# Kernel optimization log

Measured on AMD Instinct MI355X. Metric: run time of the kernel, lower is better.

The kernel has to match this reference:

```python
import math
import jax, jax.numpy as jnp
import numpy as np

B, S, CNN_D, LLM_D, BR_D, H = 4, 1024, 512, 768, 1024, 16
PW, CW = 0.2, 0.15  # physics_weight, conservation_weight


def _ln(x, g, b, eps=1e-5):
    m = jnp.mean(x, axis=-1, keepdims=True)
    v = jnp.var(x, axis=-1, keepdims=True)
    return (x - m) * jax.lax.rsqrt(v + eps) * g + b


def _mha(x, wqkv, bqkv, wo, bo, h=H):
    # torch nn.MultiheadAttention (batch_first, self-attention, eval mode)
    Bb, Ss, E = x.shape
    d = E // h
    qkv = x @ wqkv.T + bqkv
    q, k, v = jnp.split(qkv, 3, axis=-1)
    sh = lambda t: t.reshape(Bb, Ss, h, d).transpose(0, 2, 1, 3)
    q, k, v = sh(q), sh(k), sh(v)
    a = jax.nn.softmax(jnp.einsum('bhqd,bhkd->bhqk', q, k) / math.sqrt(d), axis=-1)
    o = jnp.einsum('bhqk,bhkd->bhqd', a, v).transpose(0, 2, 1, 3).reshape(Bb, Ss, E)
    return o @ wo.T + bo


def _phys_attn(qx, kx, wq, bq, wk, bk, wv, bv, wo, bo, g, be, h=H):
    # PhysicsInformedAttention._physics_attention (requires Sq == Sk for the bias broadcast)
    Bb, Sq, E = qx.shape
    Sk = kx.shape[1]
    d = E // h
    Q = (qx @ wq.T + bq).reshape(Bb, Sq, h, d).transpose(0, 2, 1, 3)
    K = (kx @ wk.T + bk).reshape(Bb, Sk, h, d).transpose(0, 2, 1, 3)
    V = (kx @ wv.T + bv).reshape(Bb, Sk, h, d).transpose(0, 2, 1, 3)
    scores = jnp.einsum('bhqd,bhkd->bhqk', Q, K) / math.sqrt(d)
    energy_bias = jnp.sum(Q * K, axis=-1, keepdims=True) * PW   # [B,H,S,1]
    mass_bias = jnp.mean(Q + K, axis=-1, keepdims=True) * CW    # [B,H,S,1]
    a = jax.nn.softmax(scores + energy_bias + mass_bias, axis=-1)
    o = jnp.einsum('bhqk,bhkd->bhqd', a, V).transpose(0, 2, 1, 3).reshape(Bb, Sq, E)
    return _ln(qx + (o @ wo.T + bo), g, be)


def _bridge(x, w, b, g, be):
    # Linear -> GELU (exact) -> LayerNorm (Dropout is no-op in eval)
    return _ln(jax.nn.gelu(x @ w.T + b, approximate=False), g, be)


def setup_inputs() -> dict:
    key = jax.random.key(0)
    ks = iter(jax.random.split(key, 64))
    nrm = lambda *s: jax.random.normal(next(ks), s, jnp.float32)
    w = lambda *s: nrm(*s) * 0.02
    return dict(
        datacube=nrm(B, 5, 8, 16, 16),
        llm_features=nrm(B, S, LLM_D),
        enhanced_cnn_features=nrm(B, S, CNN_D),
        sa_wqkv=w(3 * CNN_D, CNN_D), sa_bqkv=jnp.zeros(3 * CNN_D),
        sa_wo=w(CNN_D, CNN_D), sa_bo=jnp.zeros(CNN_D),
        ta_wqkv=w(3 * CNN_D, CNN_D), ta_bqkv=jnp.zeros(3 * CNN_D),
        ta_wo=w(CNN_D, CNN_D), ta_bo=jnp.zeros(CNN_D),
        c2b_w=w(BR_D, CNN_D), c2b_b=jnp.zeros(BR_D), c2b_g=jnp.ones(BR_D), c2b_be=jnp.zeros(BR_D),
        l2b_w=w(BR_D, LLM_D), l2b_b=jnp.zeros(BR_D), l2b_g=jnp.ones(BR_D), l2b_be=jnp.zeros(BR_D),
        pq_w=w(BR_D, BR_D), pq_b=jnp.zeros(BR_D),
        pk_w=w(BR_D, BR_D), pk_b=jnp.zeros(BR_D),
        pv_w=w(BR_D, BR_D), pv_b=jnp.zeros(BR_D),
        po_w=w(BR_D, BR_D), po_b=jnp.zeros(BR_D),
        e_emb=nrm(1, 1, BR_D), m_emb=nrm(1, 1, BR_D), p_emb=nrm(1, 1, BR_D),
        pa_g=jnp.ones(BR_D), pa_be=jnp.zeros(BR_D),
        c2l_w=w(LLM_D, BR_D), c2l_b=jnp.zeros(LLM_D), c2l_g=jnp.ones(LLM_D), c2l_be=jnp.zeros(LLM_D),
        l2c_w=w(CNN_D, BR_D), l2c_b=jnp.zeros(CNN_D), l2c_g=jnp.ones(CNN_D), l2c_be=jnp.zeros(CNN_D),
    )


def reference(datacube, llm_features, enhanced_cnn_features,
              sa_wqkv, sa_bqkv, sa_wo, sa_bo,
              ta_wqkv, ta_bqkv, ta_wo, ta_bo,
              c2b_w, c2b_b, c2b_g, c2b_be,
              l2b_w, l2b_b, l2b_g, l2b_be,
              pq_w, pq_b, pk_w, pk_b, pv_w, pv_b, po_w, po_b,
              e_emb, m_emb, p_emb, pa_g, pa_be,
              c2l_w, c2l_b, c2l_g, c2l_be,
              l2c_w, l2c_b, l2c_g, l2c_be):
    # enhanced_cnn_features path bypasses the conv3d processor
    cnn = enhanced_cnn_features                       # [B,S,512]
    cnn = cnn + _mha(cnn, sa_wqkv, sa_bqkv, sa_wo, sa_bo)   # spatial integration
    cnn = cnn + _mha(cnn, ta_wqkv, ta_bqkv, ta_wo, ta_bo)   # temporal integration
    cnn_b = _bridge(cnn, c2b_w, c2b_b, c2b_g, c2b_be)       # [B,S,1024]
    llm_b = _bridge(llm_features, l2b_w, l2b_b, l2b_g, l2b_be)  # [B,S,1024]
    phys = jnp.broadcast_to(jnp.concatenate([e_emb, m_emb, p_emb], axis=1),
                            (cnn.shape[0], 3, BR_D))
    aug_cnn = jnp.concatenate([cnn_b, phys], axis=1)  # [B,S+3,1024]
    aug_llm = jnp.concatenate([llm_b, phys], axis=1)
    cnn_att = _phys_attn(aug_cnn, aug_llm, pq_w, pq_b, pk_w, pk_b, pv_w, pv_b,
                         po_w, po_b, pa_g, pa_be)[:, :S]
    llm_att = _phys_attn(aug_llm, aug_cnn, pq_w, pq_b, pk_w, pk_b, pv_w, pv_b,
                         po_w, po_b, pa_g, pa_be)[:, :S]
    llm_enhanced = _bridge(cnn_att, c2l_w, c2l_b, c2l_g, c2l_be)  # cnn->llm bridge [B,S,768]
    cnn_enhanced = _bridge(llm_att, l2c_w, l2c_b, l2c_g, l2c_be)  # llm->cnn bridge [B,S,512]
    return (cnn_enhanced, llm_enhanced)
```

## Files before the change

kernel.cpp:

```cpp
#include <hip/hip_runtime.h>
#include <cstdint>
#include <cstddef>

#define B_    4
#define S_    1024
#define CNN_DIM 512
#define LLM_DIM 768
#define BR_DIM  1024
#define NH    16
#define SAUG  1027

typedef __attribute__((ext_vector_type(8))) short short8;
typedef __attribute__((ext_vector_type(4))) float f32x4;
typedef __attribute__((ext_vector_type(4))) unsigned short us4;
typedef unsigned short u16;
typedef unsigned int u32;
typedef unsigned long long u64;

__device__ __forceinline__ float bf2f(u16 h) {
    union { u32 u; float f; } c; c.u = ((u32)h) << 16; return c.f;
}
__device__ __forceinline__ u16 f2bf(float f) {
    union { u32 u; float f; } c; c.f = f;
    return (u16)((c.u + 0x7FFFu + ((c.u >> 16) & 1u)) >> 16);
}
__device__ __forceinline__ short f2bfS(float f) { return (short)f2bf(f); }
__device__ __forceinline__ u32 cvt_pk_bf16(float lo, float hi) {
    u32 r;
    asm("v_cvt_pk_bf16_f32 %0, %1, %2" : "=v"(r) : "v"(lo), "v"(hi));
    return r;
}

#define GLLDS(gp, lp) __builtin_amdgcn_global_load_lds( \
    (const __attribute__((address_space(1))) void*)(gp), \
    (__attribute__((address_space(3))) void*)(lp), 16, 0, 0)

#define NCONV 14
struct ConvArgs { const float* src[NCONV]; u16* dst[NCONV]; int cum[NCONV + 1]; };

__global__ __launch_bounds__(256) void convert_many(ConvArgs a, int total4) {
    int idx = blockIdx.x * 256 + threadIdx.x;
    if (idx >= total4) return;
    int seg = 0;
#pragma unroll
    for (int i = 1; i < NCONV; i++) if (a.cum[i] <= idx) seg = i;
    int j = idx - a.cum[seg];
    float4 v = ((const float4*)a.src[seg])[j];
    us4 o;
    o[0] = f2bf(v.x); o[1] = f2bf(v.y); o[2] = f2bf(v.z); o[3] = f2bf(v.w);
    ((us4*)a.dst[seg])[j] = o;
}

template<int RESID>
__global__ __launch_bounds__(256) void gemm2_kernel(
    const u16* __restrict__ A, const u16* __restrict__ W,
    const float* __restrict__ bias, const void* __restrict__ residp,
    u16* __restrict__ C, int M, int N, int K)
{
    __shared__ u16 smA[2][64 * 64];
    __shared__ u16 smB[2][128 * 64];

    const int tid = threadIdx.x;
    const int lane = tid & 63;
    const int w = tid >> 6;
    const int wm = w & 1, wn = w >> 1;
    const int mi = lane & 15, g = lane >> 4;
    const int m0 = blockIdx.y * 64;
    const int n0 = blockIdx.x * 128;
    const int lrow = lane >> 3;
    const int lcol = lane & 7;

    f32x4 acc[2][4] = {};
    const int nk = K >> 6;
    int cur = 0;

    auto stage = [&](int buf, int kt) {
        const int kbase = kt * 64;
#pragma unroll
        for (int i = 0; i < 6; i++) {
            int c = w * 6 + i;
            if (c < 8) {
                int row = c * 8 + lrow;
                int col16 = lcol ^ (row & 7);
                int grow = m0 + row; if (grow > M - 1) grow = M - 1;
                GLLDS(A + (size_t)grow * K + kbase + col16 * 8, &smA[buf][c * 512]);
            } else {
                int c8 = c - 8;
                int row = c8 * 8 + lrow;
                int col16 = lcol ^ (row & 7);
                GLLDS(W + (size_t)(n0 + row) * K + kbase + col16 * 8, &smB[buf][c8 * 512]);
            }
        }
    };

    stage(0, 0);
    __syncthreads();

    for (int kt = 0; kt < nk; ++kt) {
        if (kt + 1 < nk) stage(cur ^ 1, kt + 1);
#pragma unroll
        for (int h = 0; h < 2; h++) {
            short8 af[2], bf[4];
#pragma unroll
            for (int im = 0; im < 2; im++) {
                int row = wm * 32 + im * 16 + mi;
                af[im] = *(const short8*)&smA[cur][row * 64 + ((h * 4 + g) ^ (mi & 7)) * 8];
            }
#pragma unroll
            for (int in = 0; in < 4; in++) {
                int row = wn * 64 + in * 16 + mi;
                bf[in] = *(const short8*)&smB[cur][row * 64 + ((h * 4 + g) ^ (mi & 7)) * 8];
            }
#pragma unroll
            for (int im = 0; im < 2; im++)
#pragma unroll
                for (int in = 0; in < 4; in++)
                    acc[im][in] = __builtin_amdgcn_mfma_f32_16x16x32_bf16(af[im], bf[in], acc[im][in], 0, 0, 0);
        }
        __syncthreads();
        cur ^= 1;
    }

#pragma unroll
    for (int im = 0; im < 2; im++) {
#pragma unroll
        for (int r = 0; r < 4; r++) {
            int row = m0 + wm * 32 + im * 16 + g * 4 + r;
            if (row >= M) continue;
            size_t base = (size_t)row * N;
#pragma unroll
            for (int in = 0; in < 4; in++) {
                int col = n0 + wn * 64 + in * 16 + mi;
                float v = acc[im][in][r] + bias[col];
                if (RESID == 1) v += bf2f(((const u16*)residp)[base + col]);
                if (RESID == 2) v += ((const float*)residp)[base + col];
                C[base + col] = f2bf(v);
            }
        }
    }
}

template<int DH>
__global__ __launch_bounds__(256) void transpose_v(
    const u16* __restrict__ Vin, u16* __restrict__ VTout,
    int Sk, int in_rs, long long in_bs, int KPAD)
{
    __shared__ u16 tile[64][DH + 8];
    const int tid = threadIdx.x;
    const int b = blockIdx.z, h = blockIdx.y;
    const int k0 = blockIdx.x * 64;
    const u16* src = Vin + (size_t)b * in_bs + h * DH;

    constexpr int CH = DH / 8;
    for (int i = tid; i < 64 * CH; i += 256) {
        int key = i / CH, c = i % CH;
        short8 v = {0,0,0,0,0,0,0,0};
        if (k0 + key < Sk) v = *(const short8*)(src + (size_t)(k0 + key) * in_rs + c * 8);
        *(short8*)&tile[key][c * 8] = v;
    }
    __syncthreads();

    u16* dst = VTout + ((size_t)(b * NH + h) * DH) * KPAD + k0;
    for (int i = tid; i < DH * 8; i += 256) {
        int d = i >> 3, c = i & 7;
        short8 o;
#pragma unroll
        for (int j = 0; j < 8; j++) o[j] = (short)tile[c * 8 + j][d];
        *(short8*)(dst + (size_t)d * KPAD + c * 8) = o;
    }
}

template<int DH>
__global__ __launch_bounds__(256) void attn6(
    const u16* __restrict__ Q, const u16* __restrict__ Kb,
    const u16* __restrict__ VT, u16* __restrict__ Ob,
    int Sk, int q_rs, int kv_rs, int o_rs,
    long long q_bs, long long kv_bs, long long o_bs, int KPAD, float scale)
{
    constexpr int KT = 32;
    constexpr int NDB = DH / 16;
    constexpr int NCH = DH / 32;
    constexpr int KLDP = DH + 8;
    constexpr int VLDP = 40;
    __shared__ __align__(16) u16 Kt[KT][KLDP];
    __shared__ __align__(16) u16 Vt[DH][VLDP];
    __shared__ __align__(16) u64 Px[4][16][10];

    const int tid = threadIdx.x;
    const int lane = tid & 63;
    const int w = tid >> 6;
    const int mi = lane & 15, g = lane >> 4;
    const int b = blockIdx.z, h = blockIdx.y;
    const int hoff = h * DH;
    const int qw = blockIdx.x * 64 + w * 16;
    const float sc2 = scale * 1.44269504088896f;

    int krow, kseg; bool kact;
    int vd, vks;   bool vact;
    if (DH == 64) { krow = tid >> 3; kseg = tid & 7; kact = true;
                    vd = tid >> 2;   vks = tid & 3;  vact = true; }
    else          { krow = tid >> 2; kseg = tid & 3; kact = (tid < 128);
                    vd = (tid - 128) >> 2; vks = tid & 3; vact = (tid >= 128); }

    short8 qfrag[NCH];
    {
        const u16* qs = Q + (size_t)b * q_bs + (size_t)(qw + mi) * q_rs + hoff + g * 8;
#pragma unroll
        for (int c = 0; c < NCH; c++) {
            short8 q8 = *(const short8*)(qs + 32 * c);
#pragma unroll
            for (int j = 0; j < 8; j++) q8[j] = f2bfS(bf2f((u16)q8[j]) * sc2);
            qfrag[c] = q8;
        }
    }

    const short one = (short)0x3F80;
    const short8 ones8 = {one, one, one, one, one, one, one, one};

    f32x4 acc[NDB] = {};
    f32x4 accl = {0.f, 0.f, 0.f, 0.f};
    float m = -3.0e38f;
    const u16* kbb = Kb + (size_t)b * kv_bs + hoff;
    const u16* vtb = VT + ((size_t)(b * NH + h) * DH) * KPAD;

    const int nt = (Sk + KT - 1) / KT;

    short8 kr8 = {0,0,0,0,0,0,0,0}, vr8 = {0,0,0,0,0,0,0,0};
    auto loadKV = [&](int t) {
        if (kact) {
            int key = t * KT + krow; if (key > Sk - 1) key = Sk - 1;
            kr8 = *(const short8*)(kbb + (size_t)key * kv_rs + kseg * 8);
        }
        if (vact)
            vr8 = *(const short8*)(vtb + (size_t)vd * KPAD + t * KT + vks * 8);
    };

    loadKV(0);

    for (int t = 0; t < nt; t++) {
        const int k0 = t * KT;
        const int rem = Sk - k0;
        __syncthreads();
        if (kact) *(short8*)&Kt[krow][kseg * 8] = kr8;
        if (vact) *(short8*)&Vt[vd][vks * 8] = vr8;
        __syncthreads();
        if (t + 1 < nt) loadKV(t + 1);

        f32x4 sA = {0,0,0,0}, sB = {0,0,0,0};
#pragma unroll
        for (int c = 0; c < NCH; c++) {
            short8 ka = *(const short8*)&Kt[mi][g * 8 + 32 * c];
            short8 kb = *(const short8*)&Kt[16 + mi][g * 8 + 32 * c];
            sA = __builtin_amdgcn_mfma_f32_16x16x32_bf16(ka, qfrag[c], sA, 0, 0, 0);
            sB = __builtin_amdgcn_mfma_f32_16x16x32_bf16(kb, qfrag[c], sB, 0, 0, 0);
        }
        float sa[4], sb[4];
        if (rem >= KT) {
#pragma unroll
            for (int r = 0; r < 4; r++) { sa[r] = sA[r]; sb[r] = sB[r]; }
        } else {
#pragma unroll
            for (int r = 0; r < 4; r++) {
                sa[r] = (4 * g + r < rem)      ? sA[r] : -3.0e38f;
                sb[r] = (16 + 4 * g + r < rem) ? sB[r] : -3.0e38f;
            }
        }
        float pm = fmaxf(fmaxf(fmaxf(sa[0], sa[1]), fmaxf(sa[2], sa[3])),
                         fmaxf(fmaxf(sb[0], sb[1]), fmaxf(sb[2], sb[3])));
        pm = fmaxf(pm, __shfl_xor(pm, 16));
        pm = fmaxf(pm, __shfl_xor(pm, 32));
        if (__any(pm > m)) {
            float newm = fmaxf(m, pm);
            float corr = exp2f(m - newm);
            m = newm;
            accl *= corr;
#pragma unroll
            for (int db = 0; db < NDB; db++) acc[db] *= corr;
        }

        float pa[4], pb[4];
#pragma unroll
        for (int r = 0; r < 4; r++) {
            pa[r] = exp2f(sa[r] - m);
            pb[r] = exp2f(sb[r] - m);
        }

        {
            uint2 wa, wb;
            wa.x = cvt_pk_bf16(pa[0], pa[1]);
            wa.y = cvt_pk_bf16(pa[2], pa[3]);
            wb.x = cvt_pk_bf16(pb[0], pb[1]);
            wb.y = cvt_pk_bf16(pb[2], pb[3]);
            uint2* prow = (uint2*)&Px[w][mi][0];
            prow[g] = wa;
            prow[4 + g] = wb;
        }
        short8 pfrag = *(const short8*)((const u16*)&Px[w][mi][0] + 8 * g);

        accl = __builtin_amdgcn_mfma_f32_16x16x32_bf16(ones8, pfrag, accl, 0, 0, 0);

#pragma unroll
        for (int db = 0; db < NDB; db++) {
            short8 vf = *(const short8*)&Vt[db * 16 + mi][g * 8];
            acc[db] = __builtin_amdgcn_mfma_f32_16x16x32_bf16(vf, pfrag, acc[db], 0, 0, 0);
        }
    }

    const float inv = 1.f / accl[0];
    u16* obase = Ob + (size_t)b * o_bs + (size_t)(qw + mi) * o_rs + hoff;
#pragma unroll
    for (int db = 0; db < NDB; db++)
#pragma unroll
        for (int r = 0; r < 4; r++)
            obase[db * 16 + 4 * g + r] = f2bf(acc[db][r] * inv);
}

template<bool GELU, bool RESID, bool OUTF32>
__global__ __launch_bounds__(256) void ln_kernel(
    const u16* __restrict__ X, const u16* __restrict__ resid,
    const float* __restrict__ gg, const float* __restrict__ be,
    void* __restrict__ out, int N, int rows_per_batch,
    long long resid_bs, int resid_rs, long long out_bs, int out_rs)
{
    __shared__ float buf[1024];
    __shared__ float red[2][4];
    __shared__ float stat[2];
    const int row = blockIdx.x;
    const int b = row / rows_per_batch, r = row % rows_per_batch;
    const int tid = threadIdx.x, lane = tid & 63, w = tid >> 6;
    const u16* xr = X + (size_t)row * N;
    const u16* rr = RESID ? (resid + (size_t)b * resid_bs + (size_t)r * resid_rs) : (const u16*)nullptr;

    float s = 0.f, s2 = 0.f;
    for (int i0 = tid * 4; i0 < N; i0 += 1024) {
        us4 xv = *(const us4*)(xr + i0);
        us4 rv = {0,0,0,0};
        if (RESID) rv = *(const us4*)(rr + i0);
        float4 xb;
        float* xp = &xb.x;
#pragma unroll
        for (int u = 0; u < 4; u++) {
            float x = bf2f(xv[u]);
            if (RESID) x += bf2f(rv[u]);
            if (GELU)  x = 0.5f * x * (1.f + erff(x * 0.70710678118654752f));
            xp[u] = x; s += x; s2 += x * x;
        }
        *(float4*)&buf[i0] = xb;
    }
#pragma unroll
    for (int off = 32; off; off >>= 1) { s += __shfl_xor(s, off); s2 += __shfl_xor(s2, off); }
    if (lane == 0) { red[0][w] = s; red[1][w] = s2; }
    __syncthreads();
    if (tid == 0) {
        float a = red[0][0] + red[0][1] + red[0][2] + red[0][3];
        float q = red[1][0] + red[1][1] + red[1][2] + red[1][3];
        float mean = a / N;
        float var = q / N - mean * mean;
        stat[0] = mean; stat[1] = rsqrtf(var + 1e-5f);
    }
    __syncthreads();
    const float mean = stat[0], rs = stat[1];
    const size_t obase = (size_t)b * out_bs + (size_t)r * out_rs;
    for (int i0 = tid * 4; i0 < N; i0 += 1024) {
        if (OUTF32) {
            float4 o;
            o.x = (buf[i0+0] - mean) * rs * gg[i0+0] + be[i0+0];
            o.y = (buf[i0+1] - mean) * rs * gg[i0+1] + be[i0+1];
            o.z = (buf[i0+2] - mean) * rs * gg[i0+2] + be[i0+2];
            o.w = (buf[i0+3] - mean) * rs * gg[i0+3] + be[i0+3];
            *(float4*)((float*)out + obase + i0) = o;
        } else {
            us4 o;
#pragma unroll
            for (int u = 0; u < 4; u++)
                o[u] = f2bf((buf[i0+u] - mean) * rs * gg[i0+u] + be[i0+u]);
            *(us4*)((u16*)out + obase + i0) = o;
        }
    }
}

__global__ __launch_bounds__(256) void fill_phys_kernel(
    const float* __restrict__ e, const float* __restrict__ m, const float* __restrict__ p,
    u16* __restrict__ augc, u16* __restrict__ augl)
{
    int i = blockIdx.x * 256 + threadIdx.x;
    if (i >= 3 * BR_DIM) return;
    int r = i / BR_DIM, j = i % BR_DIM;
    u16 v = f2bf((r == 0) ? e[j] : (r == 1) ? m[j] : p[j]);
#pragma unroll
    for (int b = 0; b < B_; b++) {
        size_t off = ((size_t)b * SAUG + S_ + r) * BR_DIM + j;
        augc[off] = v; augl[off] = v;
    }
}

template<int RESID>
static void gemm(hipStream_t s, const u16* A, const u16* W, const float* bias,
                 const void* resid, u16* C, int M, int N, int K)
{
    dim3 grid(N / 128, (M + 63) / 64), block(256);
    gemm2_kernel<RESID><<<grid, block, 0, s>>>(A, W, bias, resid, C, M, N, K);
}

extern "C" void kernel_launch(void* const* d_in, const int* in_sizes, int n_in,
                              void* d_out, int out_size, void* d_ws, size_t ws_size,
                              hipStream_t stream)
{
    auto F = [&](int i) { return (const float*)d_in[i]; };
    uint8_t* ws = (uint8_t*)d_ws;

    u16* W_SA_QKV = (u16*)(ws + 256);
    u16* W_SA_O   = (u16*)(ws + 1573120);
    u16* W_TA_QKV = (u16*)(ws + 2097408);
    u16* W_TA_O   = (u16*)(ws + 3670272);
    u16* W_C2B    = (u16*)(ws + 4194560);
    u16* W_L2B    = (u16*)(ws + 5243136);
    u16* W_PQ     = (u16*)(ws + 6816000);
    u16* W_PK     = (u16*)(ws + 8913152);
    u16* W_PV     = (u16*)(ws + 11010304);
    u16* W_PO     = (u16*)(ws + 13107456);
    u16* W_C2L    = (u16*)(ws + 15204608);
    u16* W_L2C    = (u16*)(ws + 16777472);
    u16* CNN_B    = (u16*)(ws + 17826048);
    u16* LLM_B    = (u16*)(ws + 22020352);
    u16* QKV      = (u16*)(ws + 28311808);
    u16* ATT      = (u16*)(ws + 40894720);
    u16* CNN1     = (u16*)(ws + 45089024);
    u16* CNN2     = (u16*)(ws + 49283328);
    u16* AUGC     = (u16*)(ws + 53477632);
    u16* AUGL     = (u16*)(ws + 61890816);
    u16* PQ       = (u16*)(ws + 70304000);
    u16* PK       = (u16*)(ws + 78717184);
    u16* PV       = (u16*)(ws + 87130368);
    u16* VT32     = CNN_B;
    u16* VT64     = CNN_B;
    u16* X8       = QKV;
    u16* OB       = QKV;
    u16* X8b      = (u16*)(ws + 36700416);
    u16* CATT     = (u16*)(ws + 45089024);
    u16* LATT     = (u16*)(ws + 53477632);
    u16* X6       = QKV;
    u16* X4       = QKV;
    float* outp   = (float*)d_out;

    ConvArgs ca;
    const float* srcs[NCONV] = { F(1), F(2), F(3), F(5), F(7), F(9), F(11),
                                 F(15), F(19), F(21), F(23), F(25), F(32), F(36) };
    u16* dsts[NCONV] = { LLM_B, CNN_B, W_SA_QKV, W_SA_O, W_TA_QKV, W_TA_O, W_C2B,
                         W_L2B, W_PQ, W_PK, W_PV, W_PO, W_C2L, W_L2C };
    const int ns[NCONV] = { 3145728, 2097152, 786432, 262144, 786432, 262144, 524288,
                            786432, 1048576, 1048576, 1048576, 1048576, 786432, 524288 };
    int cum = 0;
    for (int i = 0; i < NCONV; i++) { ca.src[i] = srcs[i]; ca.dst[i] = dsts[i]; ca.cum[i] = cum; cum += ns[i] / 4; }
    ca.cum[NCONV] = cum;
    convert_many<<<(cum + 255) / 256, 256, 0, stream>>>(ca, cum);

    const int M4 = B_ * S_;
    const int MA = B_ * SAUG;
    const float sc32 = 0.17677669529663687f;
    const float sc64 = 0.125f;
    const long long bsQKV = (long long)S_ * 3 * CNN_DIM;
    const long long bsATT = (long long)S_ * CNN_DIM;
    const long long bsAUG = (long long)SAUG * BR_DIM;
    const long long bsO   = (long long)S_ * BR_DIM;
    const int KP32 = 1024;
    const int KP64 = 1088;
    dim3 agrid(S_ / 64, NH, B_), ablock(256);
    dim3 tgrid32(16, NH, B_), tgrid64(17, NH, B_);

    gemm<0>(stream, CNN_B, W_SA_QKV, F(4), nullptr, QKV, M4, 3 * CNN_DIM, CNN_DIM);
    transpose_v<32><<<tgrid32, 256, 0, stream>>>(QKV + 2 * CNN_DIM, VT32, S_, 3 * CNN_DIM, bsQKV, KP32);
    attn6<32><<<agrid, ablock, 0, stream>>>(QKV, QKV + CNN_DIM, VT32, ATT,
        S_, 3 * CNN_DIM, 3 * CNN_DIM, CNN_DIM, bsQKV, bsQKV, bsATT, KP32, sc32);
    gemm<2>(stream, ATT, W_SA_O, F(6), F(2), CNN1, M4, CNN_DIM, CNN_DIM);

    gemm<0>(stream, CNN1, W_TA_QKV, F(8), nullptr, QKV, M4, 3 * CNN_DIM, CNN_DIM);
    transpose_v<32><<<tgrid32, 256, 0, stream>>>(QKV + 2 * CNN_DIM, VT32, S_, 3 * CNN_DIM, bsQKV, KP32);
    attn6<32><<<agrid, ablock, 0, stream>>>(QKV, QKV + CNN_DIM, VT32, ATT,
        S_, 3 * CNN_DIM, 3 * CNN_DIM, CNN_DIM, bsQKV, bsQKV, bsATT, KP32, sc32);
    gemm<1>(stream, ATT, W_TA_O, F(10), CNN1, CNN2, M4, CNN_DIM, CNN_DIM);

    gemm<0>(stream, CNN2, W_C2B, F(12), nullptr, X8, M4, BR_DIM, CNN_DIM);
    ln_kernel<true, false, false><<<M4, 256, 0, stream>>>(X8, nullptr, F(13), F(14), AUGC,
        BR_DIM, S_, 0, 0, bsAUG, BR_DIM);
    gemm<0>(stream, LLM_B, W_L2B, F(16), nullptr, X8, M4, BR_DIM, LLM_DIM);
    ln_kernel<true, false, false><<<M4, 256, 0, stream>>>(X8, nullptr, F(17), F(18), AUGL,
        BR_DIM, S_, 0, 0, bsAUG, BR_DIM);
    fill_phys_kernel<<<12, 256, 0, stream>>>(F(27), F(28), F(29), AUGC, AUGL);

    gemm<0>(stream, AUGC, W_PQ, F(20), nullptr, PQ, MA, BR_DIM, BR_DIM);
    gemm<0>(stream, AUGL, W_PK, F(22), nullptr, PK, MA, BR_DIM, BR_DIM);
    gemm<0>(stream, AUGL, W_PV, F(24), nullptr, PV, MA, BR_DIM, BR_DIM);
    transpose_v<64><<<tgrid64, 256, 0, stream>>>(PV, VT64, SAUG, BR_DIM, bsAUG, KP64);
    attn6<64><<<agrid, ablock, 0, stream>>>(PQ, PK, VT64, OB,
        SAUG, BR_DIM, BR_DIM, BR_DIM, bsAUG, bsAUG, bsO, KP64, sc64);
    gemm<0>(stream, OB, W_PO, F(26), nullptr, X8b, M4, BR_DIM, BR_DIM);
    ln_kernel<false, true, false><<<M4, 256, 0, stream>>>(X8b, AUGC, F(30), F(31), CATT,
        BR_DIM, S_, bsAUG, BR_DIM, bsO, BR_DIM);

    gemm<0>(stream, AUGC, W_PK, F(22), nullptr, PK, MA, BR_DIM, BR_DIM);
    gemm<0>(stream, AUGC, W_PV, F(24), nullptr, PV, MA, BR_DIM, BR_DIM);
    gemm<0>(stream, AUGL, W_PQ, F(20), nullptr, PQ, MA, BR_DIM, BR_DIM);
    transpose_v<64><<<tgrid64, 256, 0, stream>>>(PV, VT64, SAUG, BR_DIM, bsAUG, KP64);
    attn6<64><<<agrid, ablock, 0, stream>>>(PQ, PK, VT64, OB,
        SAUG, BR_DIM, BR_DIM, BR_DIM, bsAUG, bsAUG, bsO, KP64, sc64);
    gemm<0>(stream, OB, W_PO, F(26), nullptr, X8b, M4, BR_DIM, BR_DIM);
    ln_kernel<false, true, false><<<M4, 256, 0, stream>>>(X8b, AUGL, F(30), F(31), LATT,
        BR_DIM, S_, bsAUG, BR_DIM, bsO, BR_DIM);

    gemm<0>(stream, CATT, W_C2L, F(33), nullptr, X6, M4, LLM_DIM, BR_DIM);
    ln_kernel<true, false, true><<<M4, 256, 0, stream>>>(X6, nullptr, F(34), F(35),
        (void*)(outp + 2097152), LLM_DIM, S_, 0, 0, (long long)S_ * LLM_DIM, LLM_DIM);
    gemm<0>(stream, LATT, W_L2C, F(37), nullptr, X4, M4, CNN_DIM, BR_DIM);
    ln_kernel<true, false, true><<<M4, 256, 0, stream>>>(X4, nullptr, F(38), F(39),
        (void*)outp, CNN_DIM, S_, 0, 0, (long long)S_ * CNN_DIM, CNN_DIM);
}
```

Measured before the change: 538.7 us.

## Batch both physics-attention directions into single launches and drop softmax max tracking

Each shared projection (Q, K, V, O) now runs as one GEMM over both augmented inputs, which sit contiguously in memory, instead of two. One attention launch with a doubled batch grid pairs each query block with the other modality's K/V, and one LayerNorm launch covers both outputs. The attention kernel also drops the online-softmax running max, rescaling and cross-lane reductions, and exponentiates raw scaled scores. This saves launches and per-tile work, but exp2 overflow becomes possible if scores are ever large. Buffer aliasing in the workspace is reworked to fit the combined tensors.

Result: faster. 471.4 us (-12.5%).

```diff
diff --git a/kernel.cpp b/kernel.cpp
--- a/kernel.cpp
+++ b/kernel.cpp
@@ -140,16 +140,16 @@
     }
 }
 
-template<int DH>
+template<int DH, bool SPLIT>
 __global__ __launch_bounds__(256) void transpose_v(
-    const u16* __restrict__ Vin, u16* __restrict__ VTout,
+    const u16* __restrict__ Vin, u16* __restrict__ VTa, u16* __restrict__ VTb,
     int Sk, int in_rs, long long in_bs, int KPAD)
 {
     __shared__ u16 tile[64][DH + 8];
     const int tid = threadIdx.x;
-    const int b = blockIdx.z, h = blockIdx.y;
+    const int gb = blockIdx.z, h = blockIdx.y;
     const int k0 = blockIdx.x * 64;
-    const u16* src = Vin + (size_t)b * in_bs + h * DH;
+    const u16* src = Vin + (size_t)gb * in_bs + h * DH;
 
     constexpr int CH = DH / 8;
     for (int i = tid; i < 64 * CH; i += 256) {
@@ -160,7 +160,11 @@
     }
     __syncthreads();
 
-    u16* dst = VTout + ((size_t)(b * NH + h) * DH) * KPAD + k0;
+    u16* base;
+    if (SPLIT) base = (gb < 4) ? (VTa + ((size_t)(gb * NH + h) * DH) * KPAD)
+                               : (VTb + ((size_t)((gb - 4) * NH + h) * DH) * KPAD);
+    else       base = VTa + ((size_t)(gb * NH + h) * DH) * KPAD;
+    u16* dst = base + k0;
     for (int i = tid; i < DH * 8; i += 256) {
         int d = i >> 3, c = i & 7;
         short8 o;
@@ -170,11 +174,11 @@
     }
 }
 
-template<int DH>
-__global__ __launch_bounds__(256) void attn6(
+template<int DH, bool PHYS>
+__global__ __launch_bounds__(256) void attn7(
     const u16* __restrict__ Q, const u16* __restrict__ Kb,
-    const u16* __restrict__ VT, u16* __restrict__ Ob,
-    int Sk, int q_rs, int kv_rs, int o_rs,
+    const u16* __restrict__ VTa, const u16* __restrict__ VTb,
+    u16* __restrict__ Ob, int Sk, int q_rs, int kv_rs, int o_rs,
     long long q_bs, long long kv_bs, long long o_bs, int KPAD, float scale)
 {
     constexpr int KT = 32;
@@ -190,10 +194,18 @@
     const int lane = tid & 63;
     const int w = tid >> 6;
     const int mi = lane & 15, g = lane >> 4;
-    const int b = blockIdx.z, h = blockIdx.y;
+    const int z = blockIdx.z, h = blockIdx.y;
     const int hoff = h * DH;
     const int qw = blockIdx.x * 64 + w * 16;
     const float sc2 = scale * 1.44269504088896f;
+
+    int kb, vg;
+    const u16* vts;
+    if (PHYS) {
+        kb = (z < 4) ? z + 4 : z - 4;
+        vts = (z < 4) ? VTb : VTa;
+        vg = (z < 4) ? z : z - 4;
+    } else { kb = z; vts = VTa; vg = z; }
 
     int krow, kseg; bool kact;
     int vd, vks;   bool vact;
@@ -204,7 +216,7 @@
 
     short8 qfrag[NCH];
     {
-        const u16* qs = Q + (size_t)b * q_bs + (size_t)(qw + mi) * q_rs + hoff + g * 8;
+        const u16* qs = Q + (size_t)z * q_bs + (size_t)(qw + mi) * q_rs + hoff + g * 8;
 #pragma unroll
         for (int c = 0; c < NCH; c++) {
             short8 q8 = *(const short8*)(qs + 32 * c);
@@ -219,9 +231,8 @@
 
     f32x4 acc[NDB] = {};
     f32x4 accl = {0.f, 0.f, 0.f, 0.f};
-    float m = -3.0e38f;
-    const u16* kbb = Kb + (size_t)b * kv_bs + hoff;
-    const u16* vtb = VT + ((size_t)(b * NH + h) * DH) * KPAD;
+    const u16* kbb = Kb + (size_t)kb * kv_bs + hoff;
+    const u16* vtb = vts + ((size_t)(vg * NH + h) * DH) * KPAD;
 
     const int nt = (Sk + KT - 1) / KT;
 
@@ -238,8 +249,7 @@
     loadKV(0);
 
     for (int t = 0; t < nt; t++) {
-        const int k0 = t * KT;
-        const int rem = Sk - k0;
+        const int rem = Sk - t * KT;
         __syncthreads();
         if (kact) *(short8*)&Kt[krow][kseg * 8] = kr8;
         if (vact) *(short8*)&Vt[vd][vks * 8] = vr8;
@@ -250,39 +260,24 @@
 #pragma unroll
         for (int c = 0; c < NCH; c++) {
             short8 ka = *(const short8*)&Kt[mi][g * 8 + 32 * c];
-            short8 kb = *(const short8*)&Kt[16 + mi][g * 8 + 32 * c];
+            short8 kb8 = *(const short8*)&Kt[16 + mi][g * 8 + 32 * c];
             sA = __builtin_amdgcn_mfma_f32_16x16x32_bf16(ka, qfrag[c], sA, 0, 0, 0);
-            sB = __builtin_amdgcn_mfma_f32_16x16x32_bf16(kb, qfrag[c], sB, 0, 0, 0);
-        }
-        float sa[4], sb[4];
+            sB = __builtin_amdgcn_mfma_f32_16x16x32_bf16(kb8, qfrag[c], sB, 0, 0, 0);
+        }
+
+        float pa[4], pb[4];
         if (rem >= KT) {
 #pragma unroll
-            for (int r = 0; r < 4; r++) { sa[r] = sA[r]; sb[r] = sB[r]; }
+            for (int r = 0; r < 4; r++) {
+                pa[r] = exp2f(sA[r]);
+                pb[r] = exp2f(sB[r]);
+            }
         } else {
 #pragma unroll
             for (int r = 0; r < 4; r++) {
-                sa[r] = (4 * g + r < rem)      ? sA[r] : -3.0e38f;
-                sb[r] = (16 + 4 * g + r < rem) ? sB[r] : -3.0e38f;
+                pa[r] = (4 * g + r < rem)      ? exp2f(sA[r]) : 0.f;
+                pb[r] = (16 + 4 * g + r < rem) ? exp2f(sB[r]) : 0.f;
             }
-        }
-        float pm = fmaxf(fmaxf(fmaxf(sa[0], sa[1]), fmaxf(sa[2], sa[3])),
-                         fmaxf(fmaxf(sb[0], sb[1]), fmaxf(sb[2], sb[3])));
-        pm = fmaxf(pm, __shfl_xor(pm, 16));
-        pm = fmaxf(pm, __shfl_xor(pm, 32));
-        if (__any(pm > m)) {
-            float newm = fmaxf(m, pm);
-            float corr = exp2f(m - newm);
-            m = newm;
-            accl *= corr;
-#pragma unroll
-            for (int db = 0; db < NDB; db++) acc[db] *= corr;
-        }
-
-        float pa[4], pb[4];
-#pragma unroll
-        for (int r = 0; r < 4; r++) {
-            pa[r] = exp2f(sa[r] - m);
-            pb[r] = exp2f(sb[r] - m);
         }
 
         {
@@ -307,7 +302,7 @@
     }
 
     const float inv = 1.f / accl[0];
-    u16* obase = Ob + (size_t)b * o_bs + (size_t)(qw + mi) * o_rs + hoff;
+    u16* obase = Ob + (size_t)z * o_bs + (size_t)(qw + mi) * o_rs + hoff;
 #pragma unroll
     for (int db = 0; db < NDB; db++)
 #pragma unroll
@@ -421,6 +416,7 @@
     u16* W_PO     = (u16*)(ws + 13107456);
     u16* W_C2L    = (u16*)(ws + 15204608);
     u16* W_L2C    = (u16*)(ws + 16777472);
+    u16* VT32     = (u16*)(ws + 17826048);
     u16* CNN_B    = (u16*)(ws + 17826048);
     u16* LLM_B    = (u16*)(ws + 22020352);
     u16* QKV      = (u16*)(ws + 28311808);
@@ -429,18 +425,17 @@
     u16* CNN2     = (u16*)(ws + 49283328);
     u16* AUGC     = (u16*)(ws + 53477632);
     u16* AUGL     = (u16*)(ws + 61890816);
-    u16* PQ       = (u16*)(ws + 70304000);
-    u16* PK       = (u16*)(ws + 78717184);
-    u16* PV       = (u16*)(ws + 87130368);
-    u16* VT32     = CNN_B;
-    u16* VT64     = CNN_B;
+    u16* VTA      = (u16*)(ws + 17826048);
+    u16* PV_ALL   = (u16*)(ws + 26738944);
+    u16* VTB      = (u16*)(ws + 43565312);
+    u16* OB_ALL   = (u16*)(ws + 26738944);
+    u16* PQ_ALL   = (u16*)(ws + 70304000);
+    u16* PK_ALL   = (u16*)(ws + 87130368);
     u16* X8       = QKV;
-    u16* OB       = QKV;
-    u16* X8b      = (u16*)(ws + 36700416);
-    u16* CATT     = (u16*)(ws + 45089024);
-    u16* LATT     = (u16*)(ws + 53477632);
-    u16* X6       = QKV;
-    u16* X4       = QKV;
+    u16* X8_ALL   = (u16*)(ws + 70304000);
+    u16* CATT_ALL = (u16*)(ws + 87130368);
+    u16* X6       = (u16*)(ws + 26738944);
+    u16* X4       = (u16*)(ws + 26738944);
     float* outp   = (float*)d_out;
 
     ConvArgs ca;
@@ -465,53 +460,46 @@
     const long long bsO   = (long long)S_ * BR_DIM;
     const int KP32 = 1024;
     const int KP64 = 1088;
-    dim3 agrid(S_ / 64, NH, B_), ablock(256);
-    dim3 tgrid32(16, NH, B_), tgrid64(17, NH, B_);
+    dim3 ablock(256);
+    dim3 agrid4(S_ / 64, NH, B_), agrid8(S_ / 64, NH, 2 * B_);
+    dim3 tgrid32(16, NH, B_), tgrid64(17, NH, 2 * B_);
 
     gemm<0>(stream, CNN_B, W_SA_QKV, F(4), nullptr, QKV, M4, 3 * CNN_DIM, CNN_DIM);
-    transpose_v<32><<<tgrid32, 256, 0, stream>>>(QKV + 2 * CNN_DIM, VT32, S_, 3 * CNN_DIM, bsQKV, KP32);
-    attn6<32><<<agrid, ablock, 0, stream>>>(QKV, QKV + CNN_DIM, VT32, ATT,
+    transpose_v<32, false><<<tgrid32, 256, 0, stream>>>(QKV + 2 * CNN_DIM, VT32, nullptr, S_, 3 * CNN_DIM, bsQKV, KP32);
+    attn7<32, false><<<agrid4, ablock, 0, stream>>>(QKV, QKV + CNN_DIM, VT32, nullptr, ATT,
         S_, 3 * CNN_DIM, 3 * CNN_DIM, CNN_DIM, bsQKV, bsQKV, bsATT, KP32, sc32);
     gemm<2>(stream, ATT, W_SA_O, F(6), F(2), CNN1, M4, CNN_DIM, CNN_DIM);
 
     gemm<0>(stream, CNN1, W_TA_QKV, F(8), nullptr, QKV, M4, 3 * CNN_DIM, CNN_DIM);
-    transpose_v<32><<<tgrid32, 256, 0, stream>>>(QKV + 2 * CNN_DIM, VT32, S_, 3 * CNN_DIM, bsQKV, KP32);
-    attn6<32><<<agrid, ablock, 0, stream>>>(QKV, QKV + CNN_DIM, VT32, ATT,
+    transpose_v<32, false><<<tgrid32, 256, 0, stream>>>(QKV + 2 * CNN_DIM, VT32, nullptr, S_, 3 * CNN_DIM, bsQKV, KP32);
+    attn7<32, false><<<agrid4, ablock, 0, stream>>>(QKV, QKV + CNN_DIM, VT32, nullptr, ATT,
         S_, 3 * CNN_DIM, 3 * CNN_DIM, CNN_DIM, bsQKV, bsQKV, bsATT, KP32, sc32);
     gemm<1>(stream, ATT, W_TA_O, F(10), CNN1, CNN2, M4, CNN_DIM, CNN_DIM);
 
+    gemm<0>(stream, LLM_B, W_L2B, F(16), nullptr, X8, M4, BR_DIM, LLM_DIM);
+    ln_kernel<true, false, false><<<M4, 256, 0, stream>>>(X8, nullptr, F(17), F(18), AUGL,
+        BR_DIM, S_, 0, 0, bsAUG, BR_DIM);
     gemm<0>(stream, CNN2, W_C2B, F(12), nullptr, X8, M4, BR_DIM, CNN_DIM);
     ln_kernel<true, false, false><<<M4, 256, 0, stream>>>(X8, nullptr, F(13), F(14), AUGC,
         BR_DIM, S_, 0, 0, bsAUG, BR_DIM);
-    gemm<0>(stream, LLM_B, W_L2B, F(16), nullptr, X8, M4, BR_DIM, LLM_DIM);
-    ln_kernel<true, false, false><<<M4, 256, 0, stream>>>(X8, nullptr, F(17), F(18), AUGL,
-        BR_DIM, S_, 0, 0, bsAUG, BR_DIM);
     fill_phys_kernel<<<12, 256, 0, stream>>>(F(27), F(28), F(29), AUGC, AUGL);
 
-    gemm<0>(stream, AUGC, W_PQ, F(20), nullptr, PQ, MA, BR_DIM, BR_DIM);
-    gemm<0>(stream, AUGL, W_PK, F(22), nullptr, PK, MA, BR_DIM, BR_DIM);
-    gemm<0>(stream, AUGL, W_PV, F(24), nullptr, PV, MA, BR_DIM, BR_DIM);
-    transpose_v<64><<<tgrid64, 256, 0, stream>>>(PV, VT64, SAUG, BR_DIM, bsAUG, KP64);
-    attn6<64><<<agrid, ablock, 0, stream>>>(PQ, PK, VT64, OB,
+    gemm<0>(stream, AUGC, W_PQ, F(20), nullptr, PQ_ALL, 2 * MA, BR_DIM, BR_DIM);
+    gemm<0>(stream, AUGC, W_PK, F(22), nullptr, PK_ALL, 2 * MA, BR_DIM, BR_DIM);
+    gemm<0>(stream, AUGC, W_PV, F(24), nullptr, PV_ALL, 2 * MA, BR_DIM, BR_DIM);
+    transpose_v<64, true><<<tgrid64, 256, 0, stream>>>(PV_ALL, VTA, VTB, SAUG, BR_DIM, bsAUG, KP64);
+
+    attn7<64, true><<<agrid8, ablock, 0, stream>>>(PQ_ALL, PK_ALL, VTA, VTB, OB_ALL,
         SAUG, BR_DIM, BR_DIM, BR_DIM, bsAUG, bsAUG, bsO, KP64, sc64);
-    gemm<0>(stream, OB, W_PO, F(26), nullptr, X8b, M4, BR_DIM, BR_DIM);
-    ln_kernel<false, true, false><<<M4, 256, 0, stream>>>(X8b, AUGC, F(30), F(31), CATT,
+
+    gemm<0>(stream, OB_ALL, W_PO, F(26), nullptr, X8_ALL, 2 * M4, BR_DIM, BR_DIM);
+    ln_kernel<false, true, false><<<2 * M4, 256, 0, stream>>>(X8_ALL, AUGC, F(30), F(31), CATT_ALL,
         BR_DIM, S_, bsAUG, BR_DIM, bsO, BR_DIM);
 
-    gemm<0>(stream, AUGC, W_PK, F(22), nullptr, PK, MA, BR_DIM, BR_DIM);
-    gemm<0>(stream, AUGC, W_PV, F(24), nullptr, PV, MA, BR_DIM, BR_DIM);
-    gemm<0>(stream, AUGL, W_PQ, F(20), nullptr, PQ, MA, BR_DIM, BR_DIM);
-    transpose_v<64><<<tgrid64, 256, 0, stream>>>(PV, VT64, SAUG, BR_DIM, bsAUG, KP64);
-    attn6<64><<<agrid, ablock, 0, stream>>>(PQ, PK, VT64, OB,
-        SAUG, BR_DIM, BR_DIM, BR_DIM, bsAUG, bsAUG, bsO, KP64, sc64);
-    gemm<0>(stream, OB, W_PO, F(26), nullptr, X8b, M4, BR_DIM, BR_DIM);
-    ln_kernel<false, true, false><<<M4, 256, 0, stream>>>(X8b, AUGL, F(30), F(31), LATT,
-        BR_DIM, S_, bsAUG, BR_DIM, bsO, BR_DIM);
-
-    gemm<0>(stream, CATT, W_C2L, F(33), nullptr, X6, M4, LLM_DIM, BR_DIM);
+    gemm<0>(stream, CATT_ALL, W_C2L, F(33), nullptr, X6, M4, LLM_DIM, BR_DIM);
     ln_kernel<true, false, true><<<M4, 256, 0, stream>>>(X6, nullptr, F(34), F(35),
         (void*)(outp + 2097152), LLM_DIM, S_, 0, 0, (long long)S_ * LLM_DIM, LLM_DIM);
-    gemm<0>(stream, LATT, W_L2C, F(37), nullptr, X4, M4, CNN_DIM, BR_DIM);
+    gemm<0>(stream, CATT_ALL + (size_t)M4 * BR_DIM, W_L2C, F(37), nullptr, X4, M4, CNN_DIM, BR_DIM);
     ln_kernel<true, false, true><<<M4, 256, 0, stream>>>(X4, nullptr, F(38), F(39),
         (void*)outp, CNN_DIM, S_, 0, 0, (long long)S_ * CNN_DIM, CNN_DIM);
 }
```
